# Optimization experiments

Measured on AMD Instinct MI355X. Metric: run time of the kernel, lower is better.

The kernel has to match this reference:

```python
import jax, jax.numpy as jnp
import numpy as np

S, T, F, J, E, H = 1024, 64, 128, 64, 256, 4
DH = E // H


def layer_norm(x, g, b, eps=1e-10):
    m = jnp.mean(x, axis=-1, keepdims=True)
    v = jnp.mean((x - m) ** 2, axis=-1, keepdims=True)  # population var (correction=0)
    return (x - m) / jnp.sqrt(v + eps) * g + b


def mha(x, Wq, Wk, Wv):
    # x: [B, L, E]; Wq/Wk/Wv: [H, E, DH]. Non-standard: scale AFTER softmax@V.
    q = jnp.einsum('ble,hed->hbld', x, Wq)
    k = jnp.einsum('ble,hed->hbld', x, Wk)
    v = jnp.einsum('ble,hed->hbld', x, Wv)
    w = jax.nn.softmax(jnp.einsum('hbld,hbmd->hblm', q, k), axis=-1)
    o = jnp.einsum('hblm,hbmd->hbld', w, v) / jnp.sqrt(jnp.asarray(Wq.shape[-1], x.dtype))
    h, b, l, d = o.shape
    return jnp.transpose(o, (1, 2, 0, 3)).reshape(b, l, h * d)


def ffn(x, W1, b1, W2, b2):
    return jnp.maximum(x @ W1 + b1, 0.0) @ W2 + b2  # Dropout is identity in eval


def pos_encoding(t, e):
    pos = jnp.arange(t, dtype=jnp.float32)[:, None]
    two_i = jnp.floor(jnp.arange(e, dtype=jnp.float32) / 2.0) * 2.0
    div = jnp.power(jnp.float32(100004.0), two_i / e)
    pe = pos / div  # [t, e]
    pe = pe.at[:, 0::2].set(jnp.sin(pe[:, 0::2]))
    pe = pe.at[:, 1::2].set(jnp.cos(pe[:, 1::2]))
    return pe


def setup_inputs() -> dict:
    key = jax.random.key(0)
    ks = jax.random.split(key, 32)
    s = 0.02
    d = {}
    d['x'] = jax.random.normal(ks[0], (S, T, F + J), dtype=jnp.float32)
    d['gate_W'] = s * jax.random.normal(ks[1], (J, F))
    d['gate_b'] = s * jax.random.normal(ks[2], (F,))
    d['embed_W'] = s * jax.random.normal(ks[3], (F, E))
    d['ln0_g'] = 1.0 + s * jax.random.normal(ks[4], (E,))
    d['ln0_b'] = s * jax.random.normal(ks[5], (E,))
    d['intra_Wq'] = s * jax.random.normal(ks[6], (H, E, DH))
    d['intra_Wk'] = s * jax.random.normal(ks[7], (H, E, DH))
    d['intra_Wv'] = s * jax.random.normal(ks[8], (H, E, DH))
    d['intra_ln_g'] = 1.0 + s * jax.random.normal(ks[9], (E,))
    d['intra_ln_b'] = s * jax.random.normal(ks[10], (E,))
    d['intra_W1'] = s * jax.random.normal(ks[11], (E, 4 * E))
    d['intra_b1'] = s * jax.random.normal(ks[12], (4 * E,))
    d['intra_W2'] = s * jax.random.normal(ks[13], (4 * E, E))
    d['intra_b2'] = s * jax.random.normal(ks[14], (E,))
    d['inter_Wq'] = s * jax.random.normal(ks[15], (H, E, DH))
    d['inter_Wk'] = s * jax.random.normal(ks[16], (H, E, DH))
    d['inter_Wv'] = s * jax.random.normal(ks[17], (H, E, DH))
    d['inter_ln1_g'] = 1.0 + s * jax.random.normal(ks[18], (E,))
    d['inter_ln1_b'] = s * jax.random.normal(ks[19], (E,))
    d['inter_ln2_g'] = 1.0 + s * jax.random.normal(ks[20], (E,))
    d['inter_ln2_b'] = s * jax.random.normal(ks[21], (E,))
    d['inter_W1'] = s * jax.random.normal(ks[22], (E, 4 * E))
    d['inter_b1'] = s * jax.random.normal(ks[23], (4 * E,))
    d['inter_W2'] = s * jax.random.normal(ks[24], (4 * E, E))
    d['inter_b2'] = s * jax.random.normal(ks[25], (E,))
    d['temp_W'] = s * jax.random.normal(ks[26], (E, E))
    d['pred_W'] = s * jax.random.normal(ks[27], (E, 1))
    d['pred_b'] = s * jax.random.normal(ks[28], (1,))
    return d


def reference(x, gate_W, gate_b, embed_W, ln0_g, ln0_b,
              intra_Wq, intra_Wk, intra_Wv, intra_ln_g, intra_ln_b,
              intra_W1, intra_b1, intra_W2, intra_b2,
              inter_Wq, inter_Wk, inter_Wv, inter_ln1_g, inter_ln1_b,
              inter_ln2_g, inter_ln2_b, inter_W1, inter_b1, inter_W2, inter_b2,
              temp_W, pred_W, pred_b):
    # Gating
    x_f = x[..., :F]                       # [S, T, F]
    x_g = x[..., -1, F:]                   # [S, J]
    gate = jax.nn.softmax(x_g @ gate_W + gate_b, axis=-1)[:, None, :]
    x_f = gate * x_f
    # Embed + positional encoding + LN
    emb = x_f @ embed_W                    # [S, T, E]
    res = emb + pos_encoding(T, E)
    ln = layer_norm(res, ln0_g, ln0_b)
    # Intra-stock attention (attend over time axis per stock)
    a = mha(ln, intra_Wq, intra_Wk, intra_Wv)
    r = a + ln
    intra_out = r + ffn(layer_norm(r, intra_ln_g, intra_ln_b), intra_W1, intra_b1, intra_W2, intra_b2)
    # Inter-stock attention (attend over stock axis per timestep)
    xT = jnp.transpose(intra_out, (1, 0, 2))            # [T, S, E]
    xTn = layer_norm(xT, inter_ln1_g, inter_ln1_b)
    a2 = mha(xTn, inter_Wq, inter_Wk, inter_Wv)          # [T, S, E]
    out = jnp.transpose(a2, (1, 0, 2))                   # [S, T, E]
    r2 = out + intra_out
    inter_out = r2 + ffn(layer_norm(r2, inter_ln2_g, inter_ln2_b), inter_W1, inter_b1, inter_W2, inter_b2)
    # Temporal aggregation
    x1 = inter_out @ temp_W                              # [S, T, E]
    cur = x1[..., -1, :][..., :, None]                   # [S, E, 1]
    lam = jax.nn.softmax(jnp.squeeze(x1 @ cur, -1), axis=-1)[:, None, :]  # [S, 1, T]
    agg = jnp.squeeze(lam @ inter_out, -2)               # [S, E]
    # Prediction
    return agg @ pred_W + pred_b                         # [S, 1]
```

## Files before the change

### kernel.cpp

```cpp
#include <hip/hip_runtime.h>


typedef _Float16 h16;
typedef __attribute__((ext_vector_type(8))) _Float16 f16x8;
typedef __attribute__((ext_vector_type(4))) _Float16 f16x4;
typedef __attribute__((ext_vector_type(4))) float f32x4;

__device__ inline float wave_sum(float v){
  #pragma unroll
  for (int o=32;o;o>>=1) v += __shfl_xor(v,o);
  return v;
}
__device__ inline float wave_max(float v){
  #pragma unroll
  for (int o=32;o;o>>=1) v = fmaxf(v,__shfl_xor(v,o));
  return v;
}

__global__ __launch_bounds__(256) void k_pe(float* __restrict__ pe){
  int t = blockIdx.x, i = threadIdx.x;
  float two_i = (float)((i>>1)<<1);
  float dv = powf(100004.0f, two_i*(1.0f/256.0f));
  float v = (float)t / dv;
  pe[t*256+i] = (i&1) ? cosf(v) : sinf(v);
}

__global__ __launch_bounds__(64) void k_gate(const float* __restrict__ x,
    const float* __restrict__ gW, const float* __restrict__ gb,
    float* __restrict__ gate){
  int s = blockIdx.x, lane = threadIdx.x;
  __shared__ float xg[64];
  xg[lane] = x[((size_t)s*64+63)*192 + 128 + lane];
  __syncthreads();
  float a0 = gb[lane], a1 = gb[64+lane];
  #pragma unroll 4
  for (int j=0;j<64;j++){
    float xv = xg[j];
    a0 += xv*gW[j*128+lane];
    a1 += xv*gW[j*128+64+lane];
  }
  float mx = wave_max(fmaxf(a0,a1));
  float e0 = __expf(a0-mx), e1 = __expf(a1-mx);
  float sm = wave_sum(e0+e1);
  gate[s*128+lane]    = e0/sm;
  gate[s*128+64+lane] = e1/sm;
}

__global__ __launch_bounds__(256) void k_t16all(
    const float* __restrict__ q1, const float* __restrict__ k1, const float* __restrict__ v1,
    const float* __restrict__ q2, const float* __restrict__ k2, const float* __restrict__ v2,
    const float* __restrict__ embed_W, const float* __restrict__ temp_W,
    const float* __restrict__ iW1, const float* __restrict__ iW2,
    const float* __restrict__ eW1, const float* __restrict__ eW2,
    h16* __restrict__ base){
  __shared__ float tile[32][33];
  const int b = blockIdx.x, tid = threadIdx.x;
  const float* src; h16* dst; int K, N, tb; bool qkv = false;
  if (b < 384){
    int mat = b>>6; tb = b&63; qkv = true; K = 256; N = 256;
    src = (mat==0)?q1:(mat==1)?k1:(mat==2)?v1:(mat==3)?q2:(mat==4)?k2:v2;
    dst = base + mat*65536;
  } else if (b < 416){ tb = b-384;  K=128;  N=256;  src=embed_W; dst=base+393216; }
  else if (b < 480){ tb = b-416;  K=256;  N=256;  src=temp_W;  dst=base+425984; }
  else if (b < 736){ tb = b-480;  K=256;  N=1024; src=iW1;     dst=base+491520; }
  else if (b < 992){ tb = b-736;  K=1024; N=256;  src=iW2;     dst=base+753664; }
  else if (b < 1248){ tb = b-992; K=256;  N=1024; src=eW1;     dst=base+1015808; }
  else               { tb = b-1248; K=1024; N=256; src=eW2;    dst=base+1277952; }
  const int nt = N>>5;
  const int N0 = (tb & (nt-1))<<5;
  const int K0 = (tb/nt)<<5;
  {
    int r = tid>>3, c0 = (tid&7)<<2;
    int k = K0+r, n = N0+c0;
    const float* p = qkv ? (src + ((n>>6)<<14) + (k<<6) + (n&63))
                         : (src + (size_t)k*N + n);
    float4 v = *(const float4*)p;
    tile[r][c0]=v.x; tile[r][c0+1]=v.y; tile[r][c0+2]=v.z; tile[r][c0+3]=v.w;
  }
  __syncthreads();
  {
    int r = tid>>3, c0 = (tid&7)<<2;
    f16x4 o;
    o[0]=(h16)tile[c0][r]; o[1]=(h16)tile[c0+1][r];
    o[2]=(h16)tile[c0+2][r]; o[3]=(h16)tile[c0+3][r];
    *(f16x4*)(dst + (size_t)(N0+r)*K + K0 + c0) = o;
  }
}

__global__ __launch_bounds__(256) void k_embed(
    const float* __restrict__ x, const h16* __restrict__ Et,
    const float* __restrict__ pe, const float* __restrict__ gate,
    const float* __restrict__ g0, const float* __restrict__ b0,
    float* __restrict__ A){
  __shared__ char pool[65536];
  h16*  As  = (h16*)pool;
  float* res = (float*)pool;
  const int tid = threadIdx.x, lane = tid&63, w = tid>>6;
  const int lr = lane&15, g = lane>>4;
  const int m0 = blockIdx.x<<6;
  #pragma unroll
  for (int it=0; it<8; it++){
    int f4 = it*256 + tid;
    int row = f4>>5, c4 = (f4&31)<<2;
    float4 v = *(const float4*)(x + (size_t)(m0+row)*192 + c4);
    float4 gg = *(const float4*)(gate + (((m0+row)>>6)<<7) + c4);
    v.x*=gg.x; v.y*=gg.y; v.z*=gg.z; v.w*=gg.w;
    int idx = ((row<<7) + c4) ^ ((row&7)<<3);
    f16x4 o; o[0]=(h16)v.x; o[1]=(h16)v.y; o[2]=(h16)v.z; o[3]=(h16)v.w;
    *(f16x4*)&As[idx] = o;
  }
  __syncthreads();
  f32x4 acc[4][4];
  #pragma unroll
  for (int a=0;a<4;a++)
    #pragma unroll
    for (int b=0;b<4;b++) acc[a][b] = (f32x4){0,0,0,0};
  #pragma unroll
  for (int i=0; i<4; i++){
    int kt = (i + w) & 3;
    f16x8 af[4], bf[4];
    #pragma unroll
    for (int rf=0; rf<4; rf++){
      int r = (rf<<4) + lr;
      int idx = ((r<<7) + (kt<<5) + (g<<3)) ^ ((r&7)<<3);
      af[rf] = *(const f16x8*)&As[idx];
    }
    #pragma unroll
    for (int cf=0; cf<4; cf++){
      int n = (w<<6) + (cf<<4) + lr;
      bf[cf] = *(const f16x8*)(Et + (size_t)n*128 + (kt<<5) + (g<<3));
    }
    __builtin_amdgcn_s_setprio(1);
    #pragma unroll
    for (int rf=0; rf<4; rf++)
      #pragma unroll
      for (int cf=0; cf<4; cf++)
        acc[rf][cf] = __builtin_amdgcn_mfma_f32_16x16x32_f16(af[rf], bf[cf], acc[rf][cf], 0,0,0);
    __builtin_amdgcn_s_setprio(0);
  }
  __syncthreads();
  #pragma unroll
  for (int cf=0; cf<4; cf++){
    int col = (w<<6) + (cf<<4) + lr;
    #pragma unroll
    for (int rf=0; rf<4; rf++)
      #pragma unroll
      for (int i=0;i<4;i++){
        int r = (rf<<4) + (g<<2) + i;
        res[(r<<8) + col] = acc[rf][cf][i] + pe[(r<<8) + col];
      }
  }
  __syncthreads();
  {
    float4 gg = *(const float4*)(g0 + (lane<<2));
    float4 bb = *(const float4*)(b0 + (lane<<2));
    for (int rr=0; rr<16; rr++){
      int r = (w<<4) + rr;
      float4 v = *(float4*)&res[(r<<8) + (lane<<2)];
      float sm = wave_sum(v.x+v.y+v.z+v.w);
      float sq = wave_sum(v.x*v.x+v.y*v.y+v.z*v.z+v.w*v.w);
      float mean = sm*(1.f/256.f);
      float rs = rsqrtf(sq*(1.f/256.f) - mean*mean + 1e-10f);
      float4 o;
      o.x=(v.x-mean)*rs*gg.x+bb.x; o.y=(v.y-mean)*rs*gg.y+bb.y;
      o.z=(v.z-mean)*rs*gg.z+bb.z; o.w=(v.w-mean)*rs*gg.w+bb.w;
      *(float4*)(A + (size_t)(m0+r)*256 + (lane<<2)) = o;
    }
  }
}

__global__ __launch_bounds__(512,1) void k_intra(
    const float* __restrict__ A, const h16* __restrict__ Wqkv,
    float* __restrict__ Out){
  __shared__ h16 Xs[64*256];
  __shared__ h16 Qs[4*64*64];
  __shared__ h16 Ks[4*64*64];
  __shared__ h16 VsT[4*64*64];
  __shared__ h16 Ps[8*16*64];
  const int tid = threadIdx.x, lane = tid&63, w = tid>>6;
  const int lr = lane&15, g = lane>>4;
  const int m0 = blockIdx.x<<6;
  #pragma unroll
  for (int rr=0; rr<8; rr++){
    int r = (w<<3) + rr;
    float4 v = *(const float4*)(A + (size_t)(m0+r)*256 + (lane<<2));
    f16x4 o; o[0]=(h16)v.x; o[1]=(h16)v.y; o[2]=(h16)v.z; o[3]=(h16)v.w;
    int idx = ((r<<8) + (lane<<2)) ^ ((r&7)<<3);
    *(f16x4*)&Xs[idx] = o;
  }

  f32x4 aqk[2][2][4];
  f32x4 av[4][2];
  #pragma unroll
  for (int m=0;m<2;m++)
    #pragma unroll
    for (int cf=0;cf<2;cf++)
      #pragma unroll
      for (int mf=0;mf<4;mf++) aqk[m][cf][mf] = (f32x4){0,0,0,0};
  #pragma unroll
  for (int rf=0;rf<4;rf++){ av[rf][0]=(f32x4){0,0,0,0}; av[rf][1]=(f32x4){0,0,0,0}; }

  f16x8 wp[3][2];
  #pragma unroll
  for (int m=0;m<3;m++)
    #pragma unroll
    for (int cf=0;cf<2;cf++){
      int n = (w<<5) + (cf<<4) + lr;
      wp[m][cf] = *(const f16x8*)(Wqkv + (size_t)m*65536 + (size_t)n*256 + (g<<3));
    }
  __syncthreads();

  #pragma unroll
  for (int kt=0; kt<8; kt++){
    f16x8 xf[4], wf[3][2];
    #pragma unroll
    for (int m=0;m<3;m++)
      #pragma unroll
      for (int cf=0;cf<2;cf++) wf[m][cf] = wp[m][cf];
    if (kt<7){
      #pragma unroll
      for (int m=0;m<3;m++)
        #pragma unroll
        for (int cf=0;cf<2;cf++){
          int n = (w<<5) + (cf<<4) + lr;
          wp[m][cf] = *(const f16x8*)(Wqkv + (size_t)m*65536 + (size_t)n*256 + ((kt+1)<<5) + (g<<3));
        }
    }
    #pragma unroll
    for (int rf=0; rf<4; rf++){
      int r = (rf<<4) + lr;
      int idx = ((r<<8) + (kt<<5) + (g<<3)) ^ ((r&7)<<3);
      xf[rf] = *(const f16x8*)&Xs[idx];
    }
    __builtin_amdgcn_s_setprio(1);
    #pragma unroll
    for (int m=0;m<2;m++)
      #pragma unroll
      for (int cf=0;cf<2;cf++)
        #pragma unroll
        for (int mf=0;mf<4;mf++)
          aqk[m][cf][mf] = __builtin_amdgcn_mfma_f32_16x16x32_f16(wf[m][cf], xf[mf], aqk[m][cf][mf], 0,0,0);
    #pragma unroll
    for (int rf=0;rf<4;rf++)
      #pragma unroll
      for (int cf=0;cf<2;cf++)
        av[rf][cf] = __builtin_amdgcn_mfma_f32_16x16x32_f16(xf[rf], wf[2][cf], av[rf][cf], 0,0,0);
    __builtin_amdgcn_s_setprio(0);
  }
  #pragma unroll
  for (int cf=0; cf<2; cf++){
    int n0 = (w<<5) + (cf<<4) + (g<<2);
    int headq = n0>>6, d0 = n0&63;
    int hbq = headq<<12;
    #pragma unroll
    for (int mf=0; mf<4; mf++){
      int q = (mf<<4) + lr;
      int base = (q<<6) + (((d0>>3) ^ (q&7))<<3) + (d0&7);
      f16x4 oq, ok;
      #pragma unroll
      for (int i=0;i<4;i++){ oq[i]=(h16)aqk[0][cf][mf][i]; ok[i]=(h16)aqk[1][cf][mf][i]; }
      *(f16x4*)&Qs[hbq + base] = oq;
      *(f16x4*)&Ks[hbq + base] = ok;
    }
    int nv = (w<<5) + (cf<<4) + lr;
    int headv = nv>>6, dv = nv&63;
    int hbv = headv<<12;
    int vkey = (dv + (dv>>3)) & 7;
    #pragma unroll
    for (int rf=0; rf<4; rf++){
      int q0 = (rf<<4) + (g<<2);
      f16x4 ov;
      #pragma unroll
      for (int i=0;i<4;i++) ov[i]=(h16)av[rf][cf][i];
      *(f16x4*)&VsT[hbv + (dv<<6) + (((q0>>3) ^ vkey)<<3) + (q0&7)] = ov;
    }
  }
  __syncthreads();
  #pragma unroll
  for (int sl=0; sl<2; sl++){
    int slot = w + (sl<<3);
    int head = slot>>2, q0 = (slot&3)<<4;
    const int hb = head<<12;
    f16x8 qf[2];
    #pragma unroll
    for (int ks=0; ks<2; ks++)
      qf[ks] = *(const f16x8*)&Qs[hb + ((q0+lr)<<6) + (((g + (ks<<2)) ^ (lr&7))<<3)];
    f32x4 sa[4];
    #pragma unroll
    for (int mm=0;mm<4;mm++) sa[mm] = (f32x4){0,0,0,0};
    __builtin_amdgcn_s_setprio(1);
    #pragma unroll
    for (int ks=0; ks<2; ks++)
      #pragma unroll
      for (int mm=0;mm<4;mm++){
        int krow = (mm<<4) + lr;
        f16x8 af = *(const f16x8*)&Ks[hb + (krow<<6) + (((g + (ks<<2)) ^ (krow&7))<<3)];
        sa[mm] = __builtin_amdgcn_mfma_f32_16x16x32_f16(af, qf[ks], sa[mm], 0,0,0);
      }
    __builtin_amdgcn_s_setprio(0);
    float pmax = -1e30f;
    #pragma unroll
    for (int mm=0;mm<4;mm++)
      #pragma unroll
      for (int i=0;i<4;i++) pmax = fmaxf(pmax, sa[mm][i]);
    pmax = fmaxf(pmax, __shfl_xor(pmax, 16));
    pmax = fmaxf(pmax, __shfl_xor(pmax, 32));
    float ps = 0.f;
    f16x4 pv[4];
    #pragma unroll
    for (int mm=0;mm<4;mm++)
      #pragma unroll
      for (int i=0;i<4;i++){
        float p = __expf(sa[mm][i] - pmax);
        ps += p;
        pv[mm][i] = (h16)p;
      }
    ps += __shfl_xor(ps, 16);
    ps += __shfl_xor(ps, 32);
    const int pbase = w<<10;
    #pragma unroll
    for (int mm=0;mm<4;mm++){
      int k0 = (mm<<4) + (g<<2);
      int unit = k0>>3, off = k0&7;
      *(f16x4*)&Ps[pbase + (lr<<6) + ((unit ^ (lr&7))<<3) + off] = pv[mm];
    }
    f32x4 oc[4];
    #pragma unroll
    for (int cf=0;cf<4;cf++) oc[cf] = (f32x4){0,0,0,0};
    __builtin_amdgcn_s_setprio(1);
    #pragma unroll
    for (int ks=0; ks<2; ks++){
      f16x8 pa = *(const f16x8*)&Ps[pbase + (lr<<6) + (((g + (ks<<2)) ^ (lr&7))<<3)];
      #pragma unroll
      for (int cf=0;cf<4;cf++){
        int d = (cf<<4) + lr;
        int key = (d + (d>>3)) & 7;
        f16x8 bf = *(const f16x8*)&VsT[hb + (d<<6) + (((g + (ks<<2)) ^ key)<<3)];
        oc[cf] = __builtin_amdgcn_mfma_f32_16x16x32_f16(pa, bf, oc[cf], 0,0,0);
      }
    }
    __builtin_amdgcn_s_setprio(0);
    float linv = 1.0f/(ps*8.0f);
    #pragma unroll
    for (int i=0;i<4;i++){
      float li = __shfl(linv, (g<<4) + (g<<2) + i);
      int row = m0 + q0 + (g<<2) + i;
      #pragma unroll
      for (int cf=0;cf<4;cf++){
        int col = (head<<6) + (cf<<4) + lr;
        size_t ga = (size_t)row*256 + col;
        Out[ga] = oc[cf][i]*li + A[ga];
      }
    }
  }
}

template<bool DOLN>
__global__ __launch_bounds__(512) void k_qkv(
    const float* __restrict__ X,
    const float* __restrict__ lng, const float* __restrict__ lnb,
    const h16* __restrict__ Bt0,
    h16* __restrict__ Qh, h16* __restrict__ Kh, h16* __restrict__ Vh){
  __shared__ h16 Xs[64*256];
  const int tid = threadIdx.x, lane = tid&63, w = tid>>6;
  const int lr = lane&15, g = lane>>4;
  const int m0 = blockIdx.x<<6;
  {
    float4 gg, bb;
    if (DOLN){ gg = *(const float4*)(lng + (lane<<2)); bb = *(const float4*)(lnb + (lane<<2)); }
    #pragma unroll
    for (int rr=0; rr<8; rr++){
      int r = (w<<3) + rr;
      float4 v = *(const float4*)(X + (size_t)(m0+r)*256 + (lane<<2));
      if (DOLN){
        float sm = wave_sum(v.x+v.y+v.z+v.w);
        float sq = wave_sum(v.x*v.x+v.y*v.y+v.z*v.z+v.w*v.w);
        float mean = sm*(1.f/256.f);
        float rs = rsqrtf(sq*(1.f/256.f) - mean*mean + 1e-10f);
        v.x=(v.x-mean)*rs*gg.x+bb.x; v.y=(v.y-mean)*rs*gg.y+bb.y;
        v.z=(v.z-mean)*rs*gg.z+bb.z; v.w=(v.w-mean)*rs*gg.w+bb.w;
      }
      f16x4 o; o[0]=(h16)v.x; o[1]=(h16)v.y; o[2]=(h16)v.z; o[3]=(h16)v.w;
      int idx = ((r<<8) + (lane<<2)) ^ ((r&7)<<3);
      *(f16x4*)&Xs[idx] = o;
    }
  }
  f32x4 acc[3][4];
  #pragma unroll
  for (int m=0;m<3;m++)
    #pragma unroll
    for (int mf=0;mf<4;mf++) acc[m][mf] = (f32x4){0,0,0,0};
  f16x8 wp[2][3];
  #pragma unroll
  for (int s=0;s<2;s++){
    int kt = (s + w) & 7;
    #pragma unroll
    for (int m=0;m<3;m++){
      int n = (w<<4) + lr;
      wp[s][m] = *(const f16x8*)(Bt0 + (size_t)m*65536 + (size_t)n*256 + (kt<<5) + (g<<3));
    }
  }
  __syncthreads();
  #pragma unroll
  for (int i=0; i<8; i++){
    const int sl = i&1;
    int kt = (i + w) & 7;
    f16x8 xf[4], wfr[3];
    #pragma unroll
    for (int m=0;m<3;m++) wfr[m] = wp[sl][m];
    if (i<6){
      int ktn = ((i+2) + w) & 7;
      #pragma unroll
      for (int m=0;m<3;m++){
        int n = (w<<4) + lr;
        wp[sl][m] = *(const f16x8*)(Bt0 + (size_t)m*65536 + (size_t)n*256 + (ktn<<5) + (g<<3));
      }
    }
    #pragma unroll
    for (int mf=0; mf<4; mf++){
      int r = (mf<<4) + lr;
      int idx = ((r<<8) + (kt<<5) + (g<<3)) ^ ((r&7)<<3);
      xf[mf] = *(const f16x8*)&Xs[idx];
    }
    __builtin_amdgcn_s_setprio(1);
    #pragma unroll
    for (int m=0;m<3;m++)
      #pragma unroll
      for (int mf=0;mf<4;mf++)
        acc[m][mf] = __builtin_amdgcn_mfma_f32_16x16x32_f16(wfr[m], xf[mf], acc[m][mf], 0,0,0);
    __builtin_amdgcn_s_setprio(0);
  }
  const int n0 = (w<<4) + (g<<2);
  #pragma unroll
  for (int m=0;m<3;m++){
    h16* dst = (m==0)?Qh:(m==1)?Kh:Vh;
    #pragma unroll
    for (int mf=0; mf<4; mf++){
      int row = m0 + (mf<<4) + lr;
      f16x4 o;
      #pragma unroll
      for (int i=0;i<4;i++) o[i] = (h16)acc[m][mf][i];
      *(f16x4*)(dst + (size_t)row*128 + n0) = o;
    }
  }
}

template<int NT, int QG>
__global__ __launch_bounds__(256) void k_attn16(
    const h16* __restrict__ Qh, const h16* __restrict__ Kh, const h16* __restrict__ Vh,
    const float* __restrict__ Resid, float* __restrict__ Out, int hbase){
  __shared__ h16 Ks[64*64];
  __shared__ h16 VsT[64*64];
  __shared__ h16 Ps[4*QG*16*64];
  const int tid = threadIdx.x, lane = tid&63, w = tid>>6;
  const int lr = lane&15, g = lane>>4;
  int hh, t=0, qc=0, s=0;
  if (NT==1){ s = blockIdx.x; hh = blockIdx.y; }
  else      { hh = blockIdx.x; t = blockIdx.y; qc = blockIdx.z; }
  const int ccol = hh<<6;
  const int gcol = (hbase+hh)<<6;

  f16x8 qf[QG][2];
  #pragma unroll
  for (int grp=0; grp<QG; grp++){
    int ql = grp*64 + (w<<4) + lr;
    size_t m = (NT==1) ? ((size_t)s*64 + ql) : (((size_t)qc*(64*QG) + ql)*64 + t);
    const h16* qp = Qh + m*128 + ccol + (g<<3);
    qf[grp][0] = *(const f16x8*)qp;
    qf[grp][1] = *(const f16x8*)(qp + 32);
  }

  f32x4 oc[QG][4];
  float m_r[QG], l_r[QG];
  #pragma unroll
  for (int grp=0; grp<QG; grp++){
    #pragma unroll
    for (int cf=0;cf<4;cf++) oc[grp][cf] = (f32x4){0,0,0,0};
    m_r[grp] = -1e30f; l_r[grp] = 0.f;
  }

  for (int kb=0; kb<NT; kb++){
    __syncthreads();
    #pragma unroll
    for (int it=0; it<2; it++){
      int u = it*256 + tid;
      int row = u>>3, un = u&7;
      size_t m = (NT==1) ? ((size_t)s*64 + row) : (((size_t)kb*64 + row)*64 + t);
      f16x8 kv = *(const f16x8*)(Kh + m*128 + ccol + (un<<3));
      *(f16x8*)&Ks[(row<<6) + ((un ^ (row&7))<<3)] = kv;
      f16x8 vv = *(const f16x8*)(Vh + m*128 + ccol + (un<<3));
      #pragma unroll
      for (int j=0;j<8;j++){
        int d = (un<<3) + j;
        int key = (d + un) & 7;
        VsT[(d<<6) + ((((row>>3) ^ key))<<3) + (row&7)] = vv[j];
      }
    }
    __syncthreads();
    #pragma unroll
    for (int grp=0; grp<QG; grp++){
      f32x4 sa[4];
      #pragma unroll
      for (int mm=0;mm<4;mm++) sa[mm] = (f32x4){0,0,0,0};
      __builtin_amdgcn_s_setprio(1);
      #pragma unroll
      for (int ks=0; ks<2; ks++){
        #pragma unroll
        for (int mm=0;mm<4;mm++){
          int krow = (mm<<4) + lr;
          f16x8 af = *(const f16x8*)&Ks[(krow<<6) + (((g + (ks<<2)) ^ (krow&7))<<3)];
          sa[mm] = __builtin_amdgcn_mfma_f32_16x16x32_f16(af, qf[grp][ks], sa[mm], 0,0,0);
        }
      }
      __builtin_amdgcn_s_setprio(0);
      float pmax = -1e30f;
      #pragma unroll
      for (int mm=0;mm<4;mm++)
        #pragma unroll
        for (int i=0;i<4;i++) pmax = fmaxf(pmax, sa[mm][i]);
      pmax = fmaxf(pmax, __shfl_xor(pmax, 16));
      pmax = fmaxf(pmax, __shfl_xor(pmax, 32));
      float mn = fmaxf(m_r[grp], pmax);
      float sca = __expf(m_r[grp] - mn);
      m_r[grp] = mn;
      float ps = 0.f;
      f16x4 pv[4];
      #pragma unroll
      for (int mm=0;mm<4;mm++){
        #pragma unroll
        for (int i=0;i<4;i++){
          float p = __expf(sa[mm][i] - mn);
          ps += p;
          pv[mm][i] = (h16)p;
        }
      }
      ps += __shfl_xor(ps, 16);
      ps += __shfl_xor(ps, 32);
      l_r[grp] = l_r[grp]*sca + ps;
      const int pbase = ((w*QG + grp)<<10);
      #pragma unroll
      for (int mm=0;mm<4;mm++){
        int k0 = (mm<<4) + (g<<2);
        int unit = k0>>3, off = k0&7;
        *(f16x4*)&Ps[pbase + (lr<<6) + ((unit ^ (lr&7))<<3) + off] = pv[mm];
      }
      #pragma unroll
      for (int i=0;i<4;i++){
        float si = __shfl(sca, (g<<4) + (g<<2) + i);
        #pragma unroll
        for (int cf=0;cf<4;cf++) oc[grp][cf][i] *= si;
      }
      __builtin_amdgcn_s_setprio(1);
      #pragma unroll
      for (int ks=0; ks<2; ks++){
        f16x8 pa = *(const f16x8*)&Ps[pbase + (lr<<6) + (((g + (ks<<2)) ^ (lr&7))<<3)];
        #pragma unroll
        for (int cf=0;cf<4;cf++){
          int d = (cf<<4) + lr;
          int key = (d + (d>>3)) & 7;
          f16x8 bf = *(const f16x8*)&VsT[(d<<6) + (((g + (ks<<2)) ^ key)<<3)];
          oc[grp][cf] = __builtin_amdgcn_mfma_f32_16x16x32_f16(pa, bf, oc[grp][cf], 0,0,0);
        }
      }
      __builtin_amdgcn_s_setprio(0);
    }
  }
  #pragma unroll
  for (int grp=0; grp<QG; grp++){
    float linv = 1.0f/(l_r[grp]*8.0f);
    #pragma unroll
    for (int i=0;i<4;i++){
      float li = __shfl(linv, (g<<4) + (g<<2) + i);
      int ql = grp*64 + (w<<4) + (g<<2) + i;
      size_t m = (NT==1) ? ((size_t)s*64 + ql) : (((size_t)qc*(64*QG) + ql)*64 + t);
      #pragma unroll
      for (int cf=0;cf<4;cf++){
        int d = (cf<<4) + lr;
        size_t ga = m*256 + gcol + d;
        Out[ga] = oc[grp][cf][i]*li + Resid[ga];
      }
    }
  }
}

__global__ __launch_bounds__(512,1) void k_ffn5(
    const float* X, float* Out,
    const float* __restrict__ lng, const float* __restrict__ lnb,
    const h16* __restrict__ W1t, const float* __restrict__ b1,
    const h16* __restrict__ W2t, const float* __restrict__ b2){
  __shared__ h16 Xs[64*256];
  __shared__ h16 Hc[64*1024];
  const int tid  = threadIdx.x;
  const int lane = tid & 63;
  const int w    = tid >> 6;
  const int r0   = blockIdx.x << 6;
  const int lr   = lane & 15;
  const int g    = lane >> 4;
  {
    float4 gg = *(const float4*)(lng + (lane<<2));
    float4 bb = *(const float4*)(lnb + (lane<<2));
    #pragma unroll
    for (int rr=0; rr<8; rr++){
      int r = (w<<3) + rr;
      float4 v = *(const float4*)(X + (size_t)(r0+r)*256 + (lane<<2));
      float sm = wave_sum(v.x+v.y+v.z+v.w);
      float sq = wave_sum(v.x*v.x+v.y*v.y+v.z*v.z+v.w*v.w);
      float mean = sm*(1.f/256.f);
      float rs = rsqrtf(sq*(1.f/256.f) - mean*mean + 1e-10f);
      f16x4 o;
      o[0]=(h16)((v.x-mean)*rs*gg.x+bb.x); o[1]=(h16)((v.y-mean)*rs*gg.y+bb.y);
      o[2]=(h16)((v.z-mean)*rs*gg.z+bb.z); o[3]=(h16)((v.w-mean)*rs*gg.w+bb.w);
      int idx = ((r<<8) + (lane<<2)) ^ ((r&7)<<3);
      *(f16x4*)&Xs[idx] = o;
    }
  }
  {
    f32x4 acc1[8][4];
    #pragma unroll
    for (int a=0;a<8;a++)
      #pragma unroll
      for (int b=0;b<4;b++) acc1[a][b] = (f32x4){0,0,0,0};
    f16x8 wp[8];
    #pragma unroll
    for (int nf=0; nf<8; nf++){
      int n = (w<<7) + (nf<<4) + lr;
      wp[nf] = *(const f16x8*)(W1t + (size_t)n*256 + ((w&7)<<5) + (g<<3));
    }
    __syncthreads();
    #pragma unroll
    for (int i=0; i<8; i++){
      int kt = (i + w) & 7;
      f16x8 xf[4], wfr[8];
      #pragma unroll
      for (int nf=0; nf<8; nf++) wfr[nf] = wp[nf];
      if (i<7){
        int ktn = (i + 1 + w) & 7;
        #pragma unroll
        for (int nf=0; nf<8; nf++){
          int n = (w<<7) + (nf<<4) + lr;
          wp[nf] = *(const f16x8*)(W1t + (size_t)n*256 + (ktn<<5) + (g<<3));
        }
      }
      #pragma unroll
      for (int mf=0; mf<4; mf++){
        int r = (mf<<4) + lr;
        int idx = ((r<<8) + (kt<<5) + (g<<3)) ^ ((r&7)<<3);
        xf[mf] = *(const f16x8*)&Xs[idx];
      }
      __builtin_amdgcn_s_setprio(1);
      #pragma unroll
      for (int nf=0; nf<8; nf++)
        #pragma unroll
        for (int mf=0; mf<4; mf++)
          acc1[nf][mf] = __builtin_amdgcn_mfma_f32_16x16x32_f16(
              wfr[nf], xf[mf], acc1[nf][mf], 0, 0, 0);
      __builtin_amdgcn_s_setprio(0);
    }
    #pragma unroll
    for (int nf=0; nf<8; nf++){
      int n0 = (w<<7) + (nf<<4) + (g<<2);
      float4 bq = *(const float4*)(b1 + n0);
      #pragma unroll
      for (int mf=0; mf<4; mf++){
        int m = (mf<<4) + lr;
        f16x4 o;
        o[0]=(h16)fmaxf(acc1[nf][mf][0]+bq.x,0.f);
        o[1]=(h16)fmaxf(acc1[nf][mf][1]+bq.y,0.f);
        o[2]=(h16)fmaxf(acc1[nf][mf][2]+bq.z,0.f);
        o[3]=(h16)fmaxf(acc1[nf][mf][3]+bq.w,0.f);
        *(f16x4*)&Hc[((m<<10) + n0) ^ ((m&7)<<3)] = o;
      }
    }
  }
  __syncthreads();
  f32x4 acc2[4][2];
  #pragma unroll
  for (int a=0;a<4;a++){ acc2[a][0]=(f32x4){0,0,0,0}; acc2[a][1]=(f32x4){0,0,0,0}; }
  f16x8 wp2[2][2];
  #pragma unroll
  for (int s=0;s<2;s++){
    int kt = (s + (w<<2)) & 31;
    #pragma unroll
    for (int cf=0;cf<2;cf++){
      int n = (w<<5) + (cf<<4) + lr;
      wp2[s][cf] = *(const f16x8*)(W2t + (size_t)n*1024 + (kt<<5) + (g<<3));
    }
  }
  #pragma unroll
  for (int i=0; i<32; i++){
    const int sl = i&1;
    int kt = (i + (w<<2)) & 31;
    f16x8 af[4], bf[2];
    bf[0] = wp2[sl][0]; bf[1] = wp2[sl][1];
    if (i<30){
      int ktn = ((i+2) + (w<<2)) & 31;
      #pragma unroll
      for (int cf=0;cf<2;cf++){
        int n = (w<<5) + (cf<<4) + lr;
        wp2[sl][cf] = *(const f16x8*)(W2t + (size_t)n*1024 + (ktn<<5) + (g<<3));
      }
    }
    #pragma unroll
    for (int rf=0; rf<4; rf++){
      int r = (rf<<4) + lr;
      int idx = ((r<<10) + (kt<<5) + (g<<3)) ^ ((r&7)<<3);
      af[rf] = *(const f16x8*)&Hc[idx];
    }
    __builtin_amdgcn_s_setprio(1);
    #pragma unroll
    for (int rf=0; rf<4; rf++)
      #pragma unroll
      for (int cf=0; cf<2; cf++)
        acc2[rf][cf] = __builtin_amdgcn_mfma_f32_16x16x32_f16(
            af[rf], bf[cf], acc2[rf][cf], 0, 0, 0);
    __builtin_amdgcn_s_setprio(0);
  }
  #pragma unroll
  for (int cf=0; cf<2; cf++){
    int col = (w<<5) + (cf<<4) + lr;
    float bv = b2[col];
    #pragma unroll
    for (int rf=0; rf<4; rf++){
      #pragma unroll
      for (int i=0;i<4;i++){
        size_t r = (size_t)r0 + (rf<<4) + (g<<2) + i;
        float res = X[r*256 + col];
        Out[r*256 + col] = acc2[rf][cf][i] + bv + res;
      }
    }
  }
}

__global__ __launch_bounds__(256) void k_head(
    const float* __restrict__ Bb, const h16* __restrict__ Tt,
    const float* __restrict__ predW, const float* __restrict__ predb,
    float* __restrict__ out){
  __shared__ h16 Xs[64*256];
  __shared__ float X1s[64*256];
  __shared__ float lam[64];
  __shared__ float red[4];
  const int tid = threadIdx.x, lane = tid&63, w = tid>>6;
  const int lr = lane&15, g = lane>>4;
  const size_t m0 = (size_t)blockIdx.x<<6;
  #pragma unroll
  for (int it=0; it<16; it++){
    int f4 = it*256 + tid;
    int row = f4>>6, c4 = (f4&63)<<2;
    float4 v = *(const float4*)(Bb + (m0+row)*256 + c4);
    int idx = ((row<<8) + c4) ^ ((row&7)<<3);
    f16x4 o; o[0]=(h16)v.x; o[1]=(h16)v.y; o[2]=(h16)v.z; o[3]=(h16)v.w;
    *(f16x4*)&Xs[idx] = o;
  }
  __syncthreads();
  f32x4 acc[4][4];
  #pragma unroll
  for (int rf=0;rf<4;rf++)
    #pragma unroll
    for (int cf=0;cf<4;cf++) acc[rf][cf] = (f32x4){0,0,0,0};
  #pragma unroll
  for (int kt=0; kt<8; kt++){
    f16x8 af[4], bf[4];
    #pragma unroll
    for (int rf=0; rf<4; rf++){
      int r = (rf<<4) + lr;
      int idx = ((r<<8) + (kt<<5) + (g<<3)) ^ ((r&7)<<3);
      af[rf] = *(const f16x8*)&Xs[idx];
    }
    #pragma unroll
    for (int cf=0; cf<4; cf++){
      int n = (w<<6) + (cf<<4) + lr;
      bf[cf] = *(const f16x8*)(Tt + (size_t)n*256 + (kt<<5) + (g<<3));
    }
    __builtin_amdgcn_s_setprio(1);
    #pragma unroll
    for (int rf=0; rf<4; rf++)
      #pragma unroll
      for (int cf=0; cf<4; cf++)
        acc[rf][cf] = __builtin_amdgcn_mfma_f32_16x16x32_f16(af[rf], bf[cf], acc[rf][cf], 0,0,0);
    __builtin_amdgcn_s_setprio(0);
  }
  #pragma unroll
  for (int cf=0; cf<4; cf++){
    int col = (w<<6) + (cf<<4) + lr;
    #pragma unroll
    for (int rf=0; rf<4; rf++)
      #pragma unroll
      for (int i=0;i<4;i++){
        int r = (rf<<4) + (g<<2) + i;
        X1s[(r<<8) + col] = acc[rf][cf][i];
      }
  }
  __syncthreads();
  float lg[16];
  for (int r=0;r<16;r++){
    int trow = (w<<4) + r;
    float4 xa = *(float4*)&X1s[(trow<<8) + (lane<<2)];
    float4 xc = *(float4*)&X1s[(63<<8) + (lane<<2)];
    lg[r] = wave_sum(xa.x*xc.x + xa.y*xc.y + xa.z*xc.z + xa.w*xc.w);
  }
  if (lane==0){
    #pragma unroll
    for (int r=0;r<16;r++) lam[(w<<4)+r] = lg[r];
  }
  __syncthreads();
  if (tid < 64){
    float v = lam[tid];
    float mx = wave_max(v);
    float p = __expf(v-mx);
    float sm = wave_sum(p);
    lam[tid] = p/sm;
  }
  __syncthreads();
  float ag = 0.f;
  for (int t=0;t<64;t++)
    ag += lam[t]*(float)Xs[((t<<8)+tid) ^ ((t&7)<<3)];
  float wsum = wave_sum(ag * predW[tid]);
  if (lane==0) red[w] = wsum;
  __syncthreads();
  if (tid==0) out[blockIdx.x] = red[0]+red[1]+red[2]+red[3] + predb[0];
}

extern "C" void kernel_launch(void* const* d_in, const int* in_sizes, int n_in,
                              void* d_out, int out_size, void* d_ws, size_t ws_size,
                              hipStream_t stream){
  const float* x       = (const float*)d_in[0];
  const float* gate_W  = (const float*)d_in[1];
  const float* gate_b  = (const float*)d_in[2];
  const float* embed_W = (const float*)d_in[3];
  const float* ln0_g   = (const float*)d_in[4];
  const float* ln0_b   = (const float*)d_in[5];
  const float* iln_g   = (const float*)d_in[9];
  const float* iln_b   = (const float*)d_in[10];
  const float* iW1     = (const float*)d_in[11];
  const float* ib1     = (const float*)d_in[12];
  const float* iW2     = (const float*)d_in[13];
  const float* ib2     = (const float*)d_in[14];
  const float* eln1_g  = (const float*)d_in[18];
  const float* eln1_b  = (const float*)d_in[19];
  const float* eln2_g  = (const float*)d_in[20];
  const float* eln2_b  = (const float*)d_in[21];
  const float* eW1     = (const float*)d_in[22];
  const float* eb1     = (const float*)d_in[23];
  const float* eW2     = (const float*)d_in[24];
  const float* eb2     = (const float*)d_in[25];
  const float* temp_W  = (const float*)d_in[26];
  const float* pred_W  = (const float*)d_in[27];
  const float* pred_b  = (const float*)d_in[28];
  float* out = (float*)d_out;

  float* pe    = (float*)d_ws;
  float* gate  = pe + 16384;
  h16* fQKV = (h16*)((char*)d_ws + ((size_t)4<<20));
  h16* fE   = fQKV + 393216;
  h16* fT   = fE + 32768;
  h16* fW1i = fT + 65536;
  h16* fW2i = fW1i + 262144;
  h16* fW1e = fW2i + 262144;
  h16* fW2e = fW1e + 262144;
  const size_t MR = (size_t)65536*256, MH = (size_t)65536*128;
  float* A  = (float*)((char*)d_ws + ((size_t)8<<20));
  float* Bb = A + MR;
  h16* Qh = (h16*)(Bb + MR);
  h16* Kh = Qh + MH;
  h16* Vh = Kh + MH;

  k_pe  <<<64,  256, 0, stream>>>(pe);
  k_gate<<<1024, 64, 0, stream>>>(x, gate_W, gate_b, gate);
  k_t16all<<<1504,256,0,stream>>>(
      (const float*)d_in[6],(const float*)d_in[7],(const float*)d_in[8],
      (const float*)d_in[15],(const float*)d_in[16],(const float*)d_in[17],
      embed_W, temp_W, iW1, iW2, eW1, eW2, fQKV);

  k_embed<<<1024,256,0,stream>>>(x, fE, pe, gate, ln0_g, ln0_b, A);

  k_intra<<<1024,512,0,stream>>>(A, fQKV, Bb);
  k_ffn5<<<1024,512,0,stream>>>(Bb, Bb, iln_g, iln_b, fW1i, ib1, fW2i, ib2);

  for (int hp=0; hp<2; hp++){
    int hb = hp*2;
    k_qkv<true><<<1024,512,0,stream>>>(Bb, eln1_g, eln1_b,
        fQKV + 3*65536 + hb*16384, Qh, Kh, Vh);
    k_attn16<16,1><<<dim3(2,64,16),256,0,stream>>>(Qh, Kh, Vh, Bb, Bb, hb);
  }
  k_ffn5<<<1024,512,0,stream>>>(Bb, Bb, eln2_g, eln2_b, fW1e, eb1, fW2e, eb2);

  k_head<<<1024,256,0,stream>>>(Bb, fT, pred_W, pred_b, out);
}
```

Measured before the change: 712.6 us.

## Compute all four inter-stock heads in one QKV and attention launch

Replaces the two-pass loop over head pairs with a single QKV projection kernel that computes all four heads (each wave now covers 32 output columns) and a single attention launch over four heads. Q/K/V buffers widen to 256 columns and reuse the freed A region plus space after Bb. The aim is to avoid re-reading the input and recomputing layer norm twice, and to halve the launch count. The cost is more accumulator registers per thread and a single-stage weight prefetch instead of the previous double-buffered prefetch.

```diff
diff --git a/kernel.cpp b/kernel.cpp
--- a/kernel.cpp
+++ b/kernel.cpp
@@ -355,8 +355,7 @@
   }
 }
 
-template<bool DOLN>
-__global__ __launch_bounds__(512) void k_qkv(
+__global__ __launch_bounds__(512) void k_qkv4(
     const float* __restrict__ X,
     const float* __restrict__ lng, const float* __restrict__ lnb,
     const h16* __restrict__ Bt0,
@@ -366,55 +365,56 @@
   const int lr = lane&15, g = lane>>4;
   const int m0 = blockIdx.x<<6;
   {
-    float4 gg, bb;
-    if (DOLN){ gg = *(const float4*)(lng + (lane<<2)); bb = *(const float4*)(lnb + (lane<<2)); }
+    float4 gg = *(const float4*)(lng + (lane<<2));
+    float4 bb = *(const float4*)(lnb + (lane<<2));
     #pragma unroll
     for (int rr=0; rr<8; rr++){
       int r = (w<<3) + rr;
       float4 v = *(const float4*)(X + (size_t)(m0+r)*256 + (lane<<2));
-      if (DOLN){
-        float sm = wave_sum(v.x+v.y+v.z+v.w);
-        float sq = wave_sum(v.x*v.x+v.y*v.y+v.z*v.z+v.w*v.w);
-        float mean = sm*(1.f/256.f);
-        float rs = rsqrtf(sq*(1.f/256.f) - mean*mean + 1e-10f);
-        v.x=(v.x-mean)*rs*gg.x+bb.x; v.y=(v.y-mean)*rs*gg.y+bb.y;
-        v.z=(v.z-mean)*rs*gg.z+bb.z; v.w=(v.w-mean)*rs*gg.w+bb.w;
-      }
+      float sm = wave_sum(v.x+v.y+v.z+v.w);
+      float sq = wave_sum(v.x*v.x+v.y*v.y+v.z*v.z+v.w*v.w);
+      float mean = sm*(1.f/256.f);
+      float rs = rsqrtf(sq*(1.f/256.f) - mean*mean + 1e-10f);
+      v.x=(v.x-mean)*rs*gg.x+bb.x; v.y=(v.y-mean)*rs*gg.y+bb.y;
+      v.z=(v.z-mean)*rs*gg.z+bb.z; v.w=(v.w-mean)*rs*gg.w+bb.w;
       f16x4 o; o[0]=(h16)v.x; o[1]=(h16)v.y; o[2]=(h16)v.z; o[3]=(h16)v.w;
       int idx = ((r<<8) + (lane<<2)) ^ ((r&7)<<3);
       *(f16x4*)&Xs[idx] = o;
     }
   }
-  f32x4 acc[3][4];
+  f32x4 acc[3][2][4];
   #pragma unroll
   for (int m=0;m<3;m++)
     #pragma unroll
-    for (int mf=0;mf<4;mf++) acc[m][mf] = (f32x4){0,0,0,0};
-  f16x8 wp[2][3];
-  #pragma unroll
-  for (int s=0;s<2;s++){
-    int kt = (s + w) & 7;
-    #pragma unroll
-    for (int m=0;m<3;m++){
-      int n = (w<<4) + lr;
-      wp[s][m] = *(const f16x8*)(Bt0 + (size_t)m*65536 + (size_t)n*256 + (kt<<5) + (g<<3));
-    }
-  }
+    for (int cf=0;cf<2;cf++)
+      #pragma unroll
+      for (int mf=0;mf<4;mf++) acc[m][cf][mf] = (f32x4){0,0,0,0};
+  f16x8 wp[3][2];
+  #pragma unroll
+  for (int m=0;m<3;m++)
+    #pragma unroll
+    for (int cf=0;cf<2;cf++){
+      int n = (w<<5) + (cf<<4) + lr;
+      wp[m][cf] = *(const f16x8*)(Bt0 + (size_t)m*65536 + (size_t)n*256 + ((w&7)<<5) + (g<<3));
+    }
   __syncthreads();
   #pragma unroll
   for (int i=0; i<8; i++){
-    const int sl = i&1;
     int kt = (i + w) & 7;
-    f16x8 xf[4], wfr[3];
-    #pragma unroll
-    for (int m=0;m<3;m++) wfr[m] = wp[sl][m];
-    if (i<6){
-      int ktn = ((i+2) + w) & 7;
-      #pragma unroll
-      for (int m=0;m<3;m++){
-        int n = (w<<4) + lr;
-        wp[sl][m] = *(const f16x8*)(Bt0 + (size_t)m*65536 + (size_t)n*256 + (ktn<<5) + (g<<3));
-      }
+    f16x8 xf[4], wfr[3][2];
+    #pragma unroll
+    for (int m=0;m<3;m++)
+      #pragma unroll
+      for (int cf=0;cf<2;cf++) wfr[m][cf] = wp[m][cf];
+    if (i<7){
+      int ktn = (i + 1 + w) & 7;
+      #pragma unroll
+      for (int m=0;m<3;m++)
+        #pragma unroll
+        for (int cf=0;cf<2;cf++){
+          int n = (w<<5) + (cf<<4) + lr;
+          wp[m][cf] = *(const f16x8*)(Bt0 + (size_t)m*65536 + (size_t)n*256 + (ktn<<5) + (g<<3));
+        }
     }
     #pragma unroll
     for (int mf=0; mf<4; mf++){
@@ -426,21 +426,26 @@
     #pragma unroll
     for (int m=0;m<3;m++)
       #pragma unroll
-      for (int mf=0;mf<4;mf++)
-        acc[m][mf] = __builtin_amdgcn_mfma_f32_16x16x32_f16(wfr[m], xf[mf], acc[m][mf], 0,0,0);
+      for (int cf=0;cf<2;cf++)
+        #pragma unroll
+        for (int mf=0;mf<4;mf++)
+          acc[m][cf][mf] = __builtin_amdgcn_mfma_f32_16x16x32_f16(wfr[m][cf], xf[mf], acc[m][cf][mf], 0,0,0);
     __builtin_amdgcn_s_setprio(0);
   }
-  const int n0 = (w<<4) + (g<<2);
   #pragma unroll
   for (int m=0;m<3;m++){
     h16* dst = (m==0)?Qh:(m==1)?Kh:Vh;
     #pragma unroll
-    for (int mf=0; mf<4; mf++){
-      int row = m0 + (mf<<4) + lr;
-      f16x4 o;
-      #pragma unroll
-      for (int i=0;i<4;i++) o[i] = (h16)acc[m][mf][i];
-      *(f16x4*)(dst + (size_t)row*128 + n0) = o;
+    for (int cf=0;cf<2;cf++){
+      int n0 = (w<<5) + (cf<<4) + (g<<2);
+      #pragma unroll
+      for (int mf=0; mf<4; mf++){
+        int row = m0 + (mf<<4) + lr;
+        f16x4 o;
+        #pragma unroll
+        for (int i=0;i<4;i++) o[i] = (h16)acc[m][cf][mf][i];
+        *(f16x4*)(dst + (size_t)row*256 + n0) = o;
+      }
     }
   }
 }
@@ -448,24 +453,21 @@
 template<int NT, int QG>
 __global__ __launch_bounds__(256) void k_attn16(
     const h16* __restrict__ Qh, const h16* __restrict__ Kh, const h16* __restrict__ Vh,
-    const float* __restrict__ Resid, float* __restrict__ Out, int hbase){
+    const float* __restrict__ Resid, float* __restrict__ Out){
   __shared__ h16 Ks[64*64];
   __shared__ h16 VsT[64*64];
   __shared__ h16 Ps[4*QG*16*64];
   const int tid = threadIdx.x, lane = tid&63, w = tid>>6;
   const int lr = lane&15, g = lane>>4;
-  int hh, t=0, qc=0, s=0;
-  if (NT==1){ s = blockIdx.x; hh = blockIdx.y; }
-  else      { hh = blockIdx.x; t = blockIdx.y; qc = blockIdx.z; }
+  const int hh = blockIdx.x, t = blockIdx.y, qc = blockIdx.z;
   const int ccol = hh<<6;
-  const int gcol = (hbase+hh)<<6;
 
   f16x8 qf[QG][2];
   #pragma unroll
   for (int grp=0; grp<QG; grp++){
     int ql = grp*64 + (w<<4) + lr;
-    size_t m = (NT==1) ? ((size_t)s*64 + ql) : (((size_t)qc*(64*QG) + ql)*64 + t);
-    const h16* qp = Qh + m*128 + ccol + (g<<3);
+    size_t m = ((size_t)qc*(64*QG) + ql)*64 + t;
+    const h16* qp = Qh + m*256 + ccol + (g<<3);
     qf[grp][0] = *(const f16x8*)qp;
     qf[grp][1] = *(const f16x8*)(qp + 32);
   }
@@ -485,10 +487,10 @@
     for (int it=0; it<2; it++){
       int u = it*256 + tid;
       int row = u>>3, un = u&7;
-      size_t m = (NT==1) ? ((size_t)s*64 + row) : (((size_t)kb*64 + row)*64 + t);
-      f16x8 kv = *(const f16x8*)(Kh + m*128 + ccol + (un<<3));
+      size_t m = ((size_t)kb*64 + row)*64 + t;
+      f16x8 kv = *(const f16x8*)(Kh + m*256 + ccol + (un<<3));
       *(f16x8*)&Ks[(row<<6) + ((un ^ (row&7))<<3)] = kv;
-      f16x8 vv = *(const f16x8*)(Vh + m*128 + ccol + (un<<3));
+      f16x8 vv = *(const f16x8*)(Vh + m*256 + ccol + (un<<3));
       #pragma unroll
       for (int j=0;j<8;j++){
         int d = (un<<3) + j;
@@ -572,11 +574,11 @@
     for (int i=0;i<4;i++){
       float li = __shfl(linv, (g<<4) + (g<<2) + i);
       int ql = grp*64 + (w<<4) + (g<<2) + i;
-      size_t m = (NT==1) ? ((size_t)s*64 + ql) : (((size_t)qc*(64*QG) + ql)*64 + t);
+      size_t m = ((size_t)qc*(64*QG) + ql)*64 + t;
       #pragma unroll
       for (int cf=0;cf<4;cf++){
         int d = (cf<<4) + lr;
-        size_t ga = m*256 + gcol + d;
+        size_t ga = m*256 + ccol + d;
         Out[ga] = oc[grp][cf][i]*li + Resid[ga];
       }
     }
@@ -857,12 +859,12 @@
   h16* fW2i = fW1i + 262144;
   h16* fW1e = fW2i + 262144;
   h16* fW2e = fW1e + 262144;
-  const size_t MR = (size_t)65536*256, MH = (size_t)65536*128;
+  const size_t MR = (size_t)65536*256;
   float* A  = (float*)((char*)d_ws + ((size_t)8<<20));
   float* Bb = A + MR;
-  h16* Qh = (h16*)(Bb + MR);
-  h16* Kh = Qh + MH;
-  h16* Vh = Kh + MH;
+  h16* Qh2 = (h16*)A;
+  h16* Kh2 = Qh2 + MR;
+  h16* Vh2 = (h16*)(Bb + MR);
 
   k_pe  <<<64,  256, 0, stream>>>(pe);
   k_gate<<<1024, 64, 0, stream>>>(x, gate_W, gate_b, gate);
@@ -876,12 +878,8 @@
   k_intra<<<1024,512,0,stream>>>(A, fQKV, Bb);
   k_ffn5<<<1024,512,0,stream>>>(Bb, Bb, iln_g, iln_b, fW1i, ib1, fW2i, ib2);
 
-  for (int hp=0; hp<2; hp++){
-    int hb = hp*2;
-    k_qkv<true><<<1024,512,0,stream>>>(Bb, eln1_g, eln1_b,
-        fQKV + 3*65536 + hb*16384, Qh, Kh, Vh);
-    k_attn16<16,1><<<dim3(2,64,16),256,0,stream>>>(Qh, Kh, Vh, Bb, Bb, hb);
-  }
+  k_qkv4<<<1024,512,0,stream>>>(Bb, eln1_g, eln1_b, fQKV + 3*65536, Qh2, Kh2, Vh2);
+  k_attn16<16,1><<<dim3(4,64,16),256,0,stream>>>(Qh2, Kh2, Vh2, Bb, Bb);
   k_ffn5<<<1024,512,0,stream>>>(Bb, Bb, eln2_g, eln2_b, fW1e, eb1, fW2e, eb2);
 
   k_head<<<1024,256,0,stream>>>(Bb, fT, pred_W, pred_b, out);
```

Result: no change. 719.9 us (+1.0%).
